# Kernel optimization log

Hardware: AMD Instinct MI355X
Metric: run time of the kernel (lower is better)

Reference implementation:

```python
import jax, jax.numpy as jnp
import numpy as np

EPS = 1e-8

def setup_inputs() -> dict:
    key = jax.random.key(0)
    ks = jax.random.split(key, 4)
    B, Cin, Cout, H, W, K, S = 16, 512, 512, 64, 64, 3, 512
    return {
        "input": jax.random.normal(ks[0], (B, Cin, H, W), jnp.float32),
        "style": jax.random.normal(ks[1], (B, S), jnp.float32),
        "weight": jax.random.normal(ks[2], (Cout, Cin, K, K), jnp.float32),
        # modulation Linear: StyleGAN2 EqualLinear with bias init 1
        "mod_w": jax.random.normal(ks[3], (Cin, S), jnp.float32) / np.sqrt(S).astype(np.float32),
        "mod_b": jnp.ones((Cin,), jnp.float32),
    }

def reference(input, style, weight, mod_w, mod_b):
    B, Cin, H, W = input.shape
    Cout, _, K, _ = weight.shape
    scale = np.float32(1.0 / np.sqrt(Cin * K * K))  # StyleGAN2 equalized-lr scale
    # modulation: Linear(style) -> per-sample per-in-channel scale
    s = style @ mod_w.T + mod_b                                  # (B, Cin)
    w = scale * weight[None] * s[:, None, :, None, None]         # (B, Cout, Cin, K, K)
    # demodulation: rsqrt of per-output-filter energy
    demod = jax.lax.rsqrt(jnp.sum(w * w, axis=(2, 3, 4)) + EPS)  # (B, Cout)
    w = w * demod[:, :, None, None, None]
    pad = K // 2
    # per-sample conv == grouped conv with groups=B in the torch original;
    # vmap over batch gives the same math without the grouped-conv trick.
    def conv_one(x, wk):
        return jax.lax.conv_general_dilated(
            x[None], wk, window_strides=(1, 1),
            padding=[(pad, pad), (pad, pad)],
            dimension_numbers=("NCHW", "OIHW", "NCHW"))[0]
    return jax.vmap(conv_one)(input, w)                          # (B, Cout, H, W)
```

## Files before the change

kernel.cpp:

```cpp
#include <hip/hip_runtime.h>

#define BATCH 16
#define CIN   512
#define COUT  512
#define HDIM  64
#define HW    4096
#define STY   512
#define NTAP  9
#define SCALE 0.014731391274719739f

typedef __bf16 bf16x8 __attribute__((ext_vector_type(8)));
typedef float  f32x4  __attribute__((ext_vector_type(4)));

static __device__ __forceinline__ unsigned short f2bf(float f) {
  union { float f; unsigned u; } v; v.f = f;
  unsigned u = v.u;
  u += 0x7fffu + ((u >> 16) & 1u);
  return (unsigned short)(u >> 16);
}

typedef const __attribute__((address_space(1))) unsigned GBUF;
typedef __attribute__((address_space(3))) unsigned LBUF;
static __device__ __forceinline__ void gload_lds16(const void* g, void* l) {
  __builtin_amdgcn_global_load_lds((GBUF*)g, (LBUF*)l, 16, 0, 0);
}

__global__ void k_style(const float* __restrict__ style, const float* __restrict__ mod_w,
                        const float* __restrict__ mod_b, float* __restrict__ S) {
  __shared__ __align__(16) float sty[STY];
  int b = blockIdx.x;
  for (int j = threadIdx.x; j < STY; j += 256) sty[j] = style[b*STY + j];
  __syncthreads();
  for (int ci = threadIdx.x; ci < CIN; ci += 256) {
    const float4* wr = reinterpret_cast<const float4*>(mod_w + ci*STY);
    const float4* sr = reinterpret_cast<const float4*>(sty);
    float acc = 0.f;
    #pragma unroll 4
    for (int j = 0; j < STY/4; ++j) {
      float4 w = wr[j], s = sr[j];
      acc += w.x*s.x + w.y*s.y + w.z*s.z + w.w*s.w;
    }
    S[b*CIN + ci] = SCALE * (acc + mod_b[ci]);
  }
}

#define XP 65
__global__ void k_xmod(const float* __restrict__ in, const float* __restrict__ S,
                       unsigned short* __restrict__ xmod) {
  __shared__ unsigned short tile[64 * XP];
  int b   = blockIdx.z;
  int h   = blockIdx.y;
  int ci0 = blockIdx.x * 64;
  int w   = threadIdx.x & 63;
  int r4  = threadIdx.x >> 6;
  const float* src = in + (size_t)(b*CIN + ci0)*HW + h*HDIM + w;
  #pragma unroll
  for (int p = 0; p < 16; ++p) {
    int row = r4 + p*4;
    float s = S[b*CIN + ci0 + row];
    tile[row*XP + w] = f2bf(src[(size_t)row*HW] * s);
  }
  __syncthreads();
  int wo = threadIdx.x >> 2;
  int c0 = (threadIdx.x & 3) * 16;
  unsigned short hb[16];
  #pragma unroll
  for (int j = 0; j < 16; ++j) hb[j] = tile[(c0+j)*XP + wo];
  uint4 o0, o1;
  o0.x = (unsigned)hb[0]  | ((unsigned)hb[1]  << 16);
  o0.y = (unsigned)hb[2]  | ((unsigned)hb[3]  << 16);
  o0.z = (unsigned)hb[4]  | ((unsigned)hb[5]  << 16);
  o0.w = (unsigned)hb[6]  | ((unsigned)hb[7]  << 16);
  o1.x = (unsigned)hb[8]  | ((unsigned)hb[9]  << 16);
  o1.y = (unsigned)hb[10] | ((unsigned)hb[11] << 16);
  o1.z = (unsigned)hb[12] | ((unsigned)hb[13] << 16);
  o1.w = (unsigned)hb[14] | ((unsigned)hb[15] << 16);
  uint4* op = reinterpret_cast<uint4*>(xmod + (((size_t)(b*HDIM + h)*HDIM + wo)*CIN + ci0 + c0));
  op[0] = o0; op[1] = o1;
}

__global__ void k_wsq_pack(const float* __restrict__ weight, float* __restrict__ wsq,
                           unsigned short* __restrict__ wpack) {
  int t  = threadIdx.x;
  int co = blockIdx.x*4 + (t >> 6);
  int g  = t & 63;
  int ci = g*8;
  const float* wp = weight + (co*CIN + ci)*NTAP;
  float w[8][9];
  #pragma unroll
  for (int j = 0; j < 8; ++j)
    #pragma unroll
    for (int tp = 0; tp < 9; ++tp) w[j][tp] = wp[j*9 + tp];
  #pragma unroll
  for (int j = 0; j < 8; ++j) {
    float ssq = 0.f;
    #pragma unroll
    for (int tp = 0; tp < 9; ++tp) ssq += w[j][tp]*w[j][tp];
    wsq[co*CIN + ci + j] = ssq;
  }
  int row = co & 127, cog = co >> 7, chunk = g >> 2, q = g & 3;
  int P = row*4 + (q ^ ((row>>1)&3));
  #pragma unroll
  for (int tp = 0; tp < 9; ++tp) {
    unsigned short h[8];
    #pragma unroll
    for (int j = 0; j < 8; ++j) h[j] = f2bf(w[j][tp]);
    uint4 pk;
    pk.x = (unsigned)h[0] | ((unsigned)h[1] << 16);
    pk.y = (unsigned)h[2] | ((unsigned)h[3] << 16);
    pk.z = (unsigned)h[4] | ((unsigned)h[5] << 16);
    pk.w = (unsigned)h[6] | ((unsigned)h[7] << 16);
    int gran = ((tp*4 + cog)*16 + chunk)*512 + P;
    *reinterpret_cast<uint4*>(wpack + gran*8) = pk;
  }
}

__global__ void k_demod(const float* __restrict__ S, const float* __restrict__ wsq,
                        float* __restrict__ D) {
  int wid  = blockIdx.x * 4 + (threadIdx.x >> 6);
  int lane = threadIdx.x & 63;
  int b  = wid >> 9;
  int co = wid & 511;
  float sum = 0.f;
  #pragma unroll
  for (int i = 0; i < CIN/64; ++i) {
    int ci = lane + i*64;
    float s = S[b*CIN + ci];
    sum += s * s * wsq[co*CIN + ci];
  }
  #pragma unroll
  for (int off = 32; off > 0; off >>= 1) sum += __shfl_down(sum, off);
  if (lane == 0) D[b*COUT + co] = rsqrtf(sum + 1e-8f);
}

#define BPAD 40
__global__ __launch_bounds__(256) void k_conv(const unsigned short* __restrict__ xmod,
                                              const unsigned short* __restrict__ wpack,
                                              const float* __restrict__ D,
                                              float* __restrict__ out) {
  const int b   = blockIdx.z;
  const int cog = blockIdx.y;
  const int co0 = cog * 128;
  const int pt  = blockIdx.x;
  const int h0  = pt * 2;

  const int tid  = threadIdx.x;
  const int lane = tid & 63;
  const int wave = tid >> 6;
  const int wm   = wave >> 1;
  const int wn   = wave & 1;
  const int l15  = lane & 15;
  const int quad = lane >> 4;

  __shared__ __align__(16) unsigned short As[2][4096];
  __shared__ __align__(16) unsigned short Bs[4 * 66 * BPAD];

  f32x4 zero = {0.f, 0.f, 0.f, 0.f};
  f32x4 acc[4][4];
  #pragma unroll
  for (int i = 0; i < 4; ++i)
    #pragma unroll
    for (int j = 0; j < 4; ++j) acc[i][j] = zero;

  if (tid < 32) {
    int row = tid >> 3, rem = tid & 7;
    int ch  = (rem >> 2) * 65;
    int ci8 = (rem & 3) * 8;
    uint4 z = {0u, 0u, 0u, 0u};
    *reinterpret_cast<uint4*>(&Bs[(row*66 + ch)*BPAD + ci8]) = z;
  }

  int pa_off[4], b_base[4];
  #pragma unroll
  for (int mt = 0; mt < 4; ++mt) {
    int row = wm*64 + mt*16 + l15;
    pa_off[mt] = (row*4 + (quad ^ ((row>>1)&3))) * 8;
  }
  #pragma unroll
  for (int nt = 0; nt < 4; ++nt) {
    int px = wn*64 + nt*16 + l15;
    int r = px >> 6, c = px & 63;
    b_base[nt] = (r*66 + c) * BPAD + quad*8;
  }

  const int srow = tid >> 6;
  const int bcol = (lane >> 2);
  const int bcg  = lane & 3;
  const int g    = h0 - 1 + srow;
  const bool inr = (g >= 0) && (g < HDIM);
  const unsigned short* xsrc =
      xmod + ((size_t)(b*HDIM + (inr ? g : 0))*HDIM + bcol)*CIN + bcg*8;

  auto ldB = [&](int ci0, uint4* lB) {
    if (inr) {
      #pragma unroll
      for (int it = 0; it < 4; ++it)
        lB[it] = *reinterpret_cast<const uint4*>(xsrc + (size_t)(it*16)*CIN + ci0);
    } else {
      uint4 z = {0u,0u,0u,0u};
      #pragma unroll
      for (int it = 0; it < 4; ++it) lB[it] = z;
    }
  };
  auto wrB = [&](const uint4* lB) {
    #pragma unroll
    for (int it = 0; it < 4; ++it)
      *reinterpret_cast<uint4*>(&Bs[(srow*66 + bcol + it*16 + 1)*BPAD + bcg*8]) = lB[it];
  };

  auto gllA = [&](int bufi, int tap, int chunk) {
    const char* gb = (const char*)wpack +
        ((size_t)(((tap*4 + cog)*16 + chunk) * 512) << 4);
    char* lb = (char*)&As[bufi][0];
    #pragma unroll
    for (int j = 0; j < 2; ++j) {
      int off = (wave*2 + j) * 1024;
      gload_lds16(gb + off + lane*16, lb + off);
    }
  };

  gllA(0, 0, 0);
  uint4 lB[4];
  ldB(0, lB);
  wrB(lB);
  __syncthreads();

  int buf = 0;
  #pragma unroll 1
  for (int chunk = 0; chunk < 16; ++chunk) {
    if (chunk < 15) ldB((chunk + 1) * 32, lB);
    #pragma unroll
    for (int t = 0; t < NTAP; ++t) {
      if (t < 8)             gllA(buf^1, t+1, chunk);
      else if (chunk < 15)   gllA(buf^1, 0,   chunk+1);
      const int toff = ((t/3)*66 + (t%3)) * BPAD;
      bf16x8 af[4], bfr[4];
      #pragma unroll
      for (int mt = 0; mt < 4; ++mt) {
        uint4 raw = *reinterpret_cast<const uint4*>(&As[buf][pa_off[mt]]);
        af[mt] = __builtin_bit_cast(bf16x8, raw);
      }
      #pragma unroll
      for (int nt = 0; nt < 4; ++nt) {
        uint4 raw = *reinterpret_cast<const uint4*>(&Bs[b_base[nt] + toff]);
        bfr[nt] = __builtin_bit_cast(bf16x8, raw);
      }
      __builtin_amdgcn_s_setprio(1);
      #pragma unroll
      for (int mt = 0; mt < 4; ++mt)
        #pragma unroll
        for (int nt = 0; nt < 4; ++nt)
          acc[mt][nt] = __builtin_amdgcn_mfma_f32_16x16x32_bf16(af[mt], bfr[nt], acc[mt][nt], 0, 0, 0);
      __builtin_amdgcn_s_setprio(0);
      __syncthreads();
      buf ^= 1;
    }
    if (chunk < 15) {
      wrB(lB);
      __syncthreads();
    }
  }

  #pragma unroll
  for (int mt = 0; mt < 4; ++mt) {
    int co = co0 + wm*64 + mt*16 + quad*4;
    float dvr[4];
    #pragma unroll
    for (int r = 0; r < 4; ++r) dvr[r] = D[b*COUT + co + r];
    #pragma unroll
    for (int nt = 0; nt < 4; ++nt) {
      int px = pt*128 + wn*64 + nt*16 + l15;
      float* op = out + ((size_t)(b*COUT + co))*HW + px;
      #pragma unroll
      for (int r = 0; r < 4; ++r) op[r*HW] = acc[mt][nt][r] * dvr[r];
    }
  }
}

extern "C" void kernel_launch(void* const* d_in, const int* in_sizes, int n_in,
                              void* d_out, int out_size, void* d_ws, size_t ws_size,
                              hipStream_t stream) {
  const float* input  = (const float*)d_in[0];
  const float* style  = (const float*)d_in[1];
  const float* weight = (const float*)d_in[2];
  const float* mod_w  = (const float*)d_in[3];
  const float* mod_b  = (const float*)d_in[4];
  float* out = (float*)d_out;

  char* ws = (char*)d_ws;
  float* S = (float*)ws;
  float* D = (float*)(ws + 32768);
  float* wsq = (float*)(ws + 65536);
  unsigned short* wpack = (unsigned short*)(ws + 1114112);
  unsigned short* xmod  = (unsigned short*)(ws + 5832704);

  k_style<<<BATCH, 256, 0, stream>>>(style, mod_w, mod_b, S);
  {
    dim3 g(CIN/64, HDIM, BATCH);
    k_xmod<<<g, 256, 0, stream>>>(input, S, xmod);
  }
  k_wsq_pack<<<COUT/4, 256, 0, stream>>>(weight, wsq, wpack);
  k_demod<<<(BATCH*COUT)/4, 256, 0, stream>>>(S, wsq, D);

  dim3 grid(HW/128, COUT/128, BATCH);
  k_conv<<<grid, 256, 0, stream>>>(xmod, wpack, D, out);
}
```

Before: 614.8 us.

## Triple-buffer weight tiles with explicit vmcnt waits and raw barriers in conv

```diff
diff --git a/kernel.cpp b/kernel.cpp
--- a/kernel.cpp
+++ b/kernel.cpp
@@ -24,6 +24,10 @@
 static __device__ __forceinline__ void gload_lds16(const void* g, void* l) {
   __builtin_amdgcn_global_load_lds((GBUF*)g, (LBUF*)l, 16, 0, 0);
 }
+
+#define BARRIER() do { asm volatile("" ::: "memory"); \
+                       __builtin_amdgcn_s_barrier();  \
+                       asm volatile("" ::: "memory"); } while (0)
 
 __global__ void k_style(const float* __restrict__ style, const float* __restrict__ mod_w,
                         const float* __restrict__ mod_b, float* __restrict__ S) {
@@ -134,10 +138,10 @@
 }
 
 #define BPAD 40
-__global__ __launch_bounds__(256) void k_conv(const unsigned short* __restrict__ xmod,
-                                              const unsigned short* __restrict__ wpack,
-                                              const float* __restrict__ D,
-                                              float* __restrict__ out) {
+__global__ __launch_bounds__(256, 3) void k_conv(const unsigned short* __restrict__ xmod,
+                                                 const unsigned short* __restrict__ wpack,
+                                                 const float* __restrict__ D,
+                                                 float* __restrict__ out) {
   const int b   = blockIdx.z;
   const int cog = blockIdx.y;
   const int co0 = cog * 128;
@@ -152,7 +156,7 @@
   const int l15  = lane & 15;
   const int quad = lane >> 4;
 
-  __shared__ __align__(16) unsigned short As[2][4096];
+  __shared__ __align__(16) unsigned short As[3][4096];
   __shared__ __align__(16) unsigned short Bs[4 * 66 * BPAD];
 
   f32x4 zero = {0.f, 0.f, 0.f, 0.f};
@@ -219,25 +223,37 @@
     }
   };
 
-  gllA(0, 0, 0);
   uint4 lB[4];
   ldB(0, lB);
+  gllA(0, 0, 0);
+  gllA(1, 1, 0);
+  asm volatile("s_waitcnt vmcnt(4)" ::: "memory");
   wrB(lB);
-  __syncthreads();
-
-  int buf = 0;
+  asm volatile("s_waitcnt lgkmcnt(0)" ::: "memory");
+  BARRIER();
+
   #pragma unroll 1
   for (int chunk = 0; chunk < 16; ++chunk) {
     if (chunk < 15) ldB((chunk + 1) * 32, lB);
     #pragma unroll
     for (int t = 0; t < NTAP; ++t) {
-      if (t < 8)             gllA(buf^1, t+1, chunk);
-      else if (chunk < 15)   gllA(buf^1, 0,   chunk+1);
+      if (t < 2) {
+        if (chunk < 15) asm volatile("s_waitcnt vmcnt(6)" ::: "memory");
+        else            asm volatile("s_waitcnt vmcnt(2)" ::: "memory");
+      } else if (t == 8) {
+        if (chunk < 15) asm volatile("s_waitcnt vmcnt(2)" ::: "memory");
+        else            asm volatile("s_waitcnt vmcnt(0)" ::: "memory");
+      } else {
+        asm volatile("s_waitcnt vmcnt(2)" ::: "memory");
+      }
+      BARRIER();
+      if (t < 7)             gllA((t+2)%3, t+2, chunk);
+      else if (chunk < 15)   gllA((t+2)%3, t-7, chunk+1);
       const int toff = ((t/3)*66 + (t%3)) * BPAD;
       bf16x8 af[4], bfr[4];
       #pragma unroll
       for (int mt = 0; mt < 4; ++mt) {
-        uint4 raw = *reinterpret_cast<const uint4*>(&As[buf][pa_off[mt]]);
+        uint4 raw = *reinterpret_cast<const uint4*>(&As[t%3][pa_off[mt]]);
         af[mt] = __builtin_bit_cast(bf16x8, raw);
       }
       #pragma unroll
@@ -252,12 +268,12 @@
         for (int nt = 0; nt < 4; ++nt)
           acc[mt][nt] = __builtin_amdgcn_mfma_f32_16x16x32_bf16(af[mt], bfr[nt], acc[mt][nt], 0, 0, 0);
       __builtin_amdgcn_s_setprio(0);
-      __syncthreads();
-      buf ^= 1;
     }
     if (chunk < 15) {
+      BARRIER();
       wrB(lB);
-      __syncthreads();
+      asm volatile("s_waitcnt lgkmcnt(0)" ::: "memory");
+      BARRIER();
     }
   }
 
```

Result: faster. 547.0 us (-11.0%).

## Stream activation rows into LDS via async global_load_lds with a ring buffer

Applied to the files above, without the earlier changes.

```diff
diff --git a/kernel.cpp b/kernel.cpp
--- a/kernel.cpp
+++ b/kernel.cpp
@@ -80,7 +80,11 @@
 }
 
 __global__ void k_wsq_pack(const float* __restrict__ weight, float* __restrict__ wsq,
-                           unsigned short* __restrict__ wpack) {
+                           unsigned short* __restrict__ wpack, uint4* __restrict__ zbuf) {
+  if (blockIdx.x == 0) {
+    uint4 z = {0u,0u,0u,0u};
+    zbuf[threadIdx.x] = z;
+  }
   int t  = threadIdx.x;
   int co = blockIdx.x*4 + (t >> 6);
   int g  = t & 63;
@@ -133,11 +137,11 @@
   if (lane == 0) D[b*COUT + co] = rsqrtf(sum + 1e-8f);
 }
 
-#define BPAD 40
-__global__ __launch_bounds__(256) void k_conv(const unsigned short* __restrict__ xmod,
-                                              const unsigned short* __restrict__ wpack,
-                                              const float* __restrict__ D,
-                                              float* __restrict__ out) {
+__global__ __launch_bounds__(256, 3) void k_conv(const unsigned short* __restrict__ xmod,
+                                                 const unsigned short* __restrict__ wpack,
+                                                 const float* __restrict__ D,
+                                                 const char* __restrict__ zbuf,
+                                                 float* __restrict__ out) {
   const int b   = blockIdx.z;
   const int cog = blockIdx.y;
   const int co0 = cog * 128;
@@ -152,8 +156,7 @@
   const int l15  = lane & 15;
   const int quad = lane >> 4;
 
-  __shared__ __align__(16) unsigned short As[2][4096];
-  __shared__ __align__(16) unsigned short Bs[4 * 66 * BPAD];
+  __shared__ __align__(16) char ldsb[49152];
 
   f32x4 zero = {0.f, 0.f, 0.f, 0.f};
   f32x4 acc[4][4];
@@ -162,104 +165,116 @@
     #pragma unroll
     for (int j = 0; j < 4; ++j) acc[i][j] = zero;
 
-  if (tid < 32) {
-    int row = tid >> 3, rem = tid & 7;
-    int ch  = (rem >> 2) * 65;
-    int ci8 = (rem & 3) * 8;
-    uint4 z = {0u, 0u, 0u, 0u};
-    *reinterpret_cast<uint4*>(&Bs[(row*66 + ch)*BPAD + ci8]) = z;
-  }
-
-  int pa_off[4], b_base[4];
+  int pa_off[4];
   #pragma unroll
   for (int mt = 0; mt < 4; ++mt) {
     int row = wm*64 + mt*16 + l15;
-    pa_off[mt] = (row*4 + (quad ^ ((row>>1)&3))) * 8;
-  }
-  #pragma unroll
-  for (int nt = 0; nt < 4; ++nt) {
-    int px = wn*64 + nt*16 + l15;
-    int r = px >> 6, c = px & 63;
-    b_base[nt] = (r*66 + c) * BPAD + quad*8;
-  }
-
-  const int srow = tid >> 6;
-  const int bcol = (lane >> 2);
-  const int bcg  = lane & 3;
-  const int g    = h0 - 1 + srow;
-  const bool inr = (g >= 0) && (g < HDIM);
-  const unsigned short* xsrc =
-      xmod + ((size_t)(b*HDIM + (inr ? g : 0))*HDIM + bcol)*CIN + bcg*8;
-
-  auto ldB = [&](int ci0, uint4* lB) {
-    if (inr) {
-      #pragma unroll
-      for (int it = 0; it < 4; ++it)
-        lB[it] = *reinterpret_cast<const uint4*>(xsrc + (size_t)(it*16)*CIN + ci0);
-    } else {
-      uint4 z = {0u,0u,0u,0u};
-      #pragma unroll
-      for (int it = 0; it < 4; ++it) lB[it] = z;
-    }
+    pa_off[mt] = (row*4 + (quad ^ ((row>>1)&3))) * 16;
+  }
+
+  int b_off[3];
+  #pragma unroll
+  for (int kw = 0; kw < 3; ++kw) {
+    int colr = l15 + kw - 1;
+    b_off[kw] = colr*64 + ((quad ^ (colr & 3)) << 4);
+  }
+  const bool m0  = (l15 == 0);
+  const bool m63 = (l15 == 15);
+  const bf16x8 z8 = __builtin_bit_cast(bf16x8, (uint4){0u,0u,0u,0u});
+
+  const int colw = wave*16 + (lane >> 2);
+  const int qeff = (lane & 3) ^ ((lane >> 2) & 3);
+  const char* xb = (const char*)xmod;
+  const char* pB0; const char* pB1; const char* pB2; const char* pB3;
+  {
+    int gr;
+    gr = h0 - 1;  pB0 = (gr >= 0 && gr < HDIM) ? xb + (size_t)(b*HDIM + gr)*65536 + colw*1024 + qeff*16
+                                               : zbuf + lane*16;
+    gr = h0;      pB1 = xb + (size_t)(b*HDIM + gr)*65536 + colw*1024 + qeff*16;
+    gr = h0 + 1;  pB2 = xb + (size_t)(b*HDIM + gr)*65536 + colw*1024 + qeff*16;
+    gr = h0 + 2;  pB3 = (gr < HDIM) ? xb + (size_t)(b*HDIM + gr)*65536 + colw*1024 + qeff*16
+                                    : zbuf + lane*16;
+  }
+
+  auto gllA = [&](int s, int tap, int chunk) {
+    const char* gb = (const char*)wpack + (size_t)(((tap*4 + cog)*16 + chunk)) * 8192;
+    char* lb = ldsb + 24576 + s*8192;
+    gload_lds16(gb + (wave*2 + 0)*1024 + lane*16, lb + (wave*2 + 0)*1024);
+    gload_lds16(gb + (wave*2 + 1)*1024 + lane*16, lb + (wave*2 + 1)*1024);
   };
-  auto wrB = [&](const uint4* lB) {
-    #pragma unroll
-    for (int it = 0; it < 4; ++it)
-      *reinterpret_cast<uint4*>(&Bs[(srow*66 + bcol + it*16 + 1)*BPAD + bcg*8]) = lB[it];
-  };
-
-  auto gllA = [&](int bufi, int tap, int chunk) {
-    const char* gb = (const char*)wpack +
-        ((size_t)(((tap*4 + cog)*16 + chunk) * 512) << 4);
-    char* lb = (char*)&As[bufi][0];
-    #pragma unroll
-    for (int j = 0; j < 2; ++j) {
-      int off = (wave*2 + j) * 1024;
-      gload_lds16(gb + off + lane*16, lb + off);
-    }
-  };
-
+
+#define GLB(L) do {                                                            \
+    int pw_ = w6 + (L); if (pw_ >= 6) pw_ -= 6;                                \
+    gload_lds16(pB##L, ldsb + (pw_ << 12) + wave*1024);                        \
+  } while (0)
+
+#define TAP(T, VC, STEADY)                                                     \
+  {                                                                            \
+    asm volatile("s_waitcnt vmcnt(" #VC ")" ::: "memory");                     \
+    __builtin_amdgcn_s_barrier();                                              \
+    asm volatile("" ::: "memory");                                             \
+    if (STEADY) {                                                              \
+      if ((T) < 7) gllA(((T)+2)%3, (T)+2, chunk);                              \
+      else         gllA(((T)+2)%3, (T)-7, chunk+1);                            \
+      if ((T) == 0) { GLB(0); GLB(1); }                                        \
+      if ((T) == 3) { GLB(2); }                                                \
+      if ((T) == 6) { GLB(3); }                                                \
+    } else if ((T) < 7) {                                                      \
+      gllA(((T)+2)%3, (T)+2, chunk);                                           \
+    }                                                                          \
+    {                                                                          \
+      const int KH = (T)/3, KW = (T)%3;                                        \
+      int pp = r6 + wn + KH; if (pp >= 6) pp -= 6;                             \
+      const char* bb = ldsb + (pp << 12);                                      \
+      bf16x8 af[4], bfr[4];                                                    \
+      _Pragma("unroll")                                                        \
+      for (int mt = 0; mt < 4; ++mt)                                           \
+        af[mt] = __builtin_bit_cast(bf16x8,                                    \
+            *reinterpret_cast<const uint4*>(ldsb + 24576 + ((T)%3)*8192 + pa_off[mt])); \
+      _Pragma("unroll")                                                        \
+      for (int nt = 0; nt < 4; ++nt)                                           \
+        bfr[nt] = __builtin_bit_cast(bf16x8,                                   \
+            *reinterpret_cast<const uint4*>(bb + b_off[KW] + nt*1024));        \
+      if (KW == 0) bfr[0] = m0  ? z8 : bfr[0];                                 \
+      if (KW == 2) bfr[3] = m63 ? z8 : bfr[3];                                 \
+      __builtin_amdgcn_s_setprio(1);                                           \
+      _Pragma("unroll")                                                        \
+      for (int mt = 0; mt < 4; ++mt)                                           \
+        _Pragma("unroll")                                                      \
+        for (int nt = 0; nt < 4; ++nt)                                         \
+          acc[mt][nt] = __builtin_amdgcn_mfma_f32_16x16x32_bf16(af[mt], bfr[nt], acc[mt][nt], 0, 0, 0); \
+      __builtin_amdgcn_s_setprio(0);                                           \
+    }                                                                          \
+  }
+
+  gload_lds16(pB0, ldsb + 0*4096 + wave*1024);
+  gload_lds16(pB1, ldsb + 1*4096 + wave*1024);
+  gload_lds16(pB2, ldsb + 2*4096 + wave*1024);
+  gload_lds16(pB3, ldsb + 3*4096 + wave*1024);
+  pB0 += 64; pB1 += 64; pB2 += 64; pB3 += 64;
   gllA(0, 0, 0);
-  uint4 lB[4];
-  ldB(0, lB);
-  wrB(lB);
-  __syncthreads();
-
-  int buf = 0;
+  gllA(1, 1, 0);
+
+  int r6 = 0;
+
   #pragma unroll 1
-  for (int chunk = 0; chunk < 16; ++chunk) {
-    if (chunk < 15) ldB((chunk + 1) * 32, lB);
-    #pragma unroll
-    for (int t = 0; t < NTAP; ++t) {
-      if (t < 8)             gllA(buf^1, t+1, chunk);
-      else if (chunk < 15)   gllA(buf^1, 0,   chunk+1);
-      const int toff = ((t/3)*66 + (t%3)) * BPAD;
-      bf16x8 af[4], bfr[4];
-      #pragma unroll
-      for (int mt = 0; mt < 4; ++mt) {
-        uint4 raw = *reinterpret_cast<const uint4*>(&As[buf][pa_off[mt]]);
-        af[mt] = __builtin_bit_cast(bf16x8, raw);
-      }
-      #pragma unroll
-      for (int nt = 0; nt < 4; ++nt) {
-        uint4 raw = *reinterpret_cast<const uint4*>(&Bs[b_base[nt] + toff]);
-        bfr[nt] = __builtin_bit_cast(bf16x8, raw);
-      }
-      __builtin_amdgcn_s_setprio(1);
-      #pragma unroll
-      for (int mt = 0; mt < 4; ++mt)
-        #pragma unroll
-        for (int nt = 0; nt < 4; ++nt)
-          acc[mt][nt] = __builtin_amdgcn_mfma_f32_16x16x32_bf16(af[mt], bfr[nt], acc[mt][nt], 0, 0, 0);
-      __builtin_amdgcn_s_setprio(0);
-      __syncthreads();
-      buf ^= 1;
-    }
-    if (chunk < 15) {
-      wrB(lB);
-      __syncthreads();
-    }
-  }
+  for (int chunk = 0; chunk < 15; ++chunk) {
+    const int w6 = (r6 + 4 >= 6) ? (r6 - 2) : (r6 + 4);
+    TAP(0,2,1) TAP(1,4,1) TAP(2,4,1)
+    TAP(3,2,1) TAP(4,3,1) TAP(5,3,1)
+    TAP(6,2,1) TAP(7,3,1) TAP(8,3,1)
+    pB0 += 64; pB1 += 64; pB2 += 64; pB3 += 64;
+    r6 = w6;
+  }
+  {
+    const int chunk = 15;
+    const int w6 = 0; (void)w6;
+    TAP(0,2,0) TAP(1,2,0) TAP(2,2,0)
+    TAP(3,2,0) TAP(4,2,0) TAP(5,2,0)
+    TAP(6,2,0) TAP(7,2,0) TAP(8,0,0)
+  }
+#undef TAP
+#undef GLB
 
   #pragma unroll
   for (int mt = 0; mt < 4; ++mt) {
@@ -292,16 +307,17 @@
   float* D = (float*)(ws + 32768);
   float* wsq = (float*)(ws + 65536);
   unsigned short* wpack = (unsigned short*)(ws + 1114112);
-  unsigned short* xmod  = (unsigned short*)(ws + 5832704);
+  char* zbuf = ws + 5832704;
+  unsigned short* xmod  = (unsigned short*)(ws + 5836800);
 
   k_style<<<BATCH, 256, 0, stream>>>(style, mod_w, mod_b, S);
   {
     dim3 g(CIN/64, HDIM, BATCH);
     k_xmod<<<g, 256, 0, stream>>>(input, S, xmod);
   }
-  k_wsq_pack<<<COUT/4, 256, 0, stream>>>(weight, wsq, wpack);
+  k_wsq_pack<<<COUT/4, 256, 0, stream>>>(weight, wsq, wpack, (uint4*)zbuf);
   k_demod<<<(BATCH*COUT)/4, 256, 0, stream>>>(S, wsq, D);
 
   dim3 grid(HW/128, COUT/128, BATCH);
-  k_conv<<<grid, 256, 0, stream>>>(xmod, wpack, D, out);
-}
+  k_conv<<<grid, 256, 0, stream>>>(xmod, wpack, D, zbuf, out);
+}
```

Measured after the change: 513.8 us. 1.2x faster.
